# Performance work log

Hardware: AMD Instinct MI355X
Metric: run time of the kernel (lower is better)

Reference implementation:

```python
import jax, jax.numpy as jnp
import numpy as np
import math

B, T, C, H, S = 2, 2048, 1024, 16, 16
HD = C // H
EPS = 1e-5


def setup_inputs() -> dict:
    key = jax.random.key(0)
    ks = jax.random.split(key, 20)
    sc = 1.0 / math.sqrt(C)
    inp = {
        "x": jax.random.normal(ks[0], (B, T, C), jnp.float32),
        # A_log_fwd: log(arange(1..S)) repeated over dim (as in __init__)
        "A_log": jnp.log(jnp.tile(jnp.arange(1, S + 1, dtype=jnp.float32), (C, 1))),
        # Linear weights stored (in, out); apply as x @ W + b
        "Wd": jax.random.normal(ks[1], (C, C), jnp.float32) * sc,
        "bd": jnp.full((C,), -3.0, jnp.float32),
        "WB": jax.random.normal(ks[2], (C, S), jnp.float32) * sc,
        "WC": jax.random.normal(ks[3], (C, S), jnp.float32) * sc,
        "Wq": jax.random.normal(ks[4], (C, C), jnp.float32) * sc,
        "bq": jnp.zeros((C,), jnp.float32),
        "Wk": jax.random.normal(ks[5], (C, C), jnp.float32) * sc,
        "bk": jnp.zeros((C,), jnp.float32),
        "Wv": jax.random.normal(ks[6], (C, C), jnp.float32) * sc,
        "bv": jnp.zeros((C,), jnp.float32),
        "Wx": jax.random.normal(ks[7], (C, C), jnp.float32) * sc,
        "bx": jnp.zeros((C,), jnp.float32),
        "Wo": jax.random.normal(ks[8], (C, C), jnp.float32) * sc,
        "bo": jnp.zeros((C,), jnp.float32),
        "ln_g": jnp.ones((C,), jnp.float32),
        "ln_b": jnp.zeros((C,), jnp.float32),
        "temp": jnp.full((1, H, 1, 1), 0.5, jnp.float32),
    }
    return inp


def _forward(x, A_log, Wd, bd, WB, WC, Wq, bq, Wk, bk, Wv, bv, Wx, bx, Wo, bo, ln_g, ln_b, temp):
    x_base = x @ Wx + bx                      # (B,T,C)
    delta = jax.nn.softplus(x @ Wd + bd)      # (B,T,C)
    B_mat = x @ WB                            # (B,T,S)
    C_mat = x @ WC                            # (B,T,S)
    A = -jnp.exp(A_log)                       # (C,S)

    def scan_fn(h, inp):
        xb_t, d_t, B_t, C_t = inp             # (B,C),(B,C),(B,S),(B,S)
        bar_A = jnp.exp(d_t[..., None] * A)   # (B,C,S)
        h = bar_A * h + (d_t * xb_t)[..., None] * B_t[:, None, :]
        y = jnp.einsum('bcs,bs->bc', h, C_t)
        return h, y

    h0 = jnp.zeros((B, C, S), x.dtype)
    xs = (jnp.swapaxes(x_base, 0, 1), jnp.swapaxes(delta, 0, 1),
          jnp.swapaxes(B_mat, 0, 1), jnp.swapaxes(C_mat, 0, 1))
    _, ys = jax.lax.scan(scan_fn, h0, xs)
    out_fwd = jnp.swapaxes(ys, 0, 1)          # (B,T,C)

    # LayerNorm(x_base + out_fwd)
    hyb = x_base + out_fwd
    mu = hyb.mean(-1, keepdims=True)
    var = hyb.var(-1, keepdims=True)
    hybrid = (hyb - mu) * jax.lax.rsqrt(var + EPS) * ln_g + ln_b

    def heads(W, b):
        return (hybrid @ W + b).reshape(B, T, H, HD).transpose(0, 2, 1, 3)

    Q, K, V = heads(Wq, bq), heads(Wk, bk), heads(Wv, bv)
    scores = jnp.einsum('bhqd,bhkd->bhqk', Q, K) / math.sqrt(HD)
    scores = scores * jax.nn.softplus(temp)
    mask = jnp.tril(jnp.ones((T, T), bool))
    scores = jnp.where(mask[None, None], scores, -jnp.inf)
    attn = jax.nn.softmax(scores, axis=-1)
    out = jnp.einsum('bhqk,bhkd->bhqd', attn, V).transpose(0, 2, 1, 3).reshape(B, T, C)
    return out @ Wo + bo


def reference(x, A_log, Wd, bd, WB, WC, Wq, bq, Wk, bk, Wv, bv, Wx, bx, Wo, bo, ln_g, ln_b, temp):
    return _forward(x, A_log, Wd, bd, WB, WC, Wq, bq, Wk, bk, Wv, bv, Wx, bx, Wo, bo, ln_g, ln_b, temp)
```

## Files before the change

### kernel.cpp

```cpp
#include <hip/hip_runtime.h>
#include <math.h>

#define B_  2
#define T_  2048
#define C_  1024
#define H_  16
#define S_  16
#define HD_ 64
#define NCH 32
#define CHL 64

typedef short  short8  __attribute__((ext_vector_type(8)));
typedef unsigned short ushort8 __attribute__((ext_vector_type(8)));
typedef unsigned short ushort4v __attribute__((ext_vector_type(4)));
typedef float  f32x4   __attribute__((ext_vector_type(4)));

__device__ __forceinline__ float softplus_f(float v) {
    return fmaxf(v, 0.f) + log1pf(__expf(-fabsf(v)));
}

__device__ __forceinline__ unsigned short f2bf(float x) {
    unsigned u = __float_as_uint(x);
    u += 0x7fffu + ((u >> 16) & 1u);
    return (unsigned short)(u >> 16);
}

__device__ __forceinline__ void gload16(const unsigned short* g,
                                        unsigned short* l)
{
    __builtin_amdgcn_global_load_lds(
        (const __attribute__((address_space(1))) unsigned int*)g,
        (__attribute__((address_space(3))) unsigned int*)l, 16, 0, 0);
}

__global__ __launch_bounds__(256) void cast_bf16(const float* __restrict__ in,
                                                 unsigned short* __restrict__ out,
                                                 int n4)
{
    int i = blockIdx.x * 256 + threadIdx.x;
    if (i >= n4) return;
    float4 v = ((const float4*)in)[i];
    ushort4v o = {f2bf(v.x), f2bf(v.y), f2bf(v.z), f2bf(v.w)};
    ((ushort4v*)out)[i] = o;
}

__device__ __forceinline__ void wtrans_body(const float* __restrict__ W,
                                            unsigned short* __restrict__ WT,
                                            int bx, int by, int tid)
{
    __shared__ float t[32][33];
    const int n0 = bx * 32, k0 = by * 32;
    const int tx = tid & 31, ty = tid >> 5;
#pragma unroll
    for (int p = 0; p < 4; ++p)
        t[ty + p * 8][tx] = W[(size_t)(k0 + ty + p * 8) * C_ + n0 + tx];
    __syncthreads();
#pragma unroll
    for (int p = 0; p < 4; ++p)
        WT[(size_t)(n0 + ty + p * 8) * C_ + k0 + tx] = f2bf(t[tx][ty + p * 8]);
}

__global__ __launch_bounds__(256) void wtrans(const float* __restrict__ W,
                                              unsigned short* __restrict__ WT)
{
    wtrans_body(W, WT, blockIdx.x, blockIdx.y, threadIdx.x);
}

__global__ __launch_bounds__(256) void wtrans_multi(
    const float* __restrict__ Wx, const float* __restrict__ Wd,
    const float* __restrict__ Wq, const float* __restrict__ Wk,
    const float* __restrict__ Wv,
    unsigned short* __restrict__ Astack, unsigned short* __restrict__ Wqkv)
{
    const float* src;
    unsigned short* dst;
    switch (blockIdx.z) {
        case 0: src = Wx; dst = Astack; break;
        case 1: src = Wd; dst = Astack + (size_t)1024 * 1024; break;
        case 2: src = Wq; dst = Wqkv; break;
        case 3: src = Wk; dst = Wqkv + (size_t)1024 * 1024; break;
        default: src = Wv; dst = Wqkv + (size_t)2048 * 1024; break;
    }
    wtrans_body(src, dst, blockIdx.x, blockIdx.y, threadIdx.x);
}

__global__ __launch_bounds__(256) void prep_misc(
    const float* __restrict__ WB, const float* __restrict__ WC,
    const float* __restrict__ bx, const float* __restrict__ bd,
    const float* __restrict__ bq, const float* __restrict__ bk,
    const float* __restrict__ bv,
    unsigned short* __restrict__ Astack, float* __restrict__ biasPD,
    float* __restrict__ biasQKV)
{
    int gid = blockIdx.x * 256 + threadIdx.x;
    if (gid < 32768) {
        int w = gid >> 14, rem = gid & 16383;
        int s = rem >> 10, k = rem & 1023;
        const float* src = w ? WC : WB;
        Astack[(size_t)(2048 + w * 16 + s) * 1024 + k] = f2bf(src[k * 16 + s]);
    } else {
        int id = gid - 32768;
        if (id < 2176) {
            biasPD[id] = id < 1024 ? bx[id] : (id < 2048 ? bd[id - 1024] : 0.f);
        } else {
            int id2 = id - 2176;
            if (id2 < 3072)
                biasQKV[id2] = id2 < 1024 ? bq[id2]
                             : (id2 < 2048 ? bk[id2 - 1024] : bv[id2 - 2048]);
        }
    }
}

__global__ __launch_bounds__(256) void gemm_mfma(
    const unsigned short* __restrict__ A, const unsigned short* __restrict__ Bm,
    const float* __restrict__ bias,
    void* __restrict__ outv, void* __restrict__ out2,
    void* __restrict__ out3, void* __restrict__ out4,
    int M, int N, int K, int lda, int mode)
{
    __shared__ __align__(16) unsigned short As[4][4096];
    __shared__ __align__(16) unsigned short Bs[4][4096];

    const int tid = threadIdx.x;
    const int w = tid >> 6, lane = tid & 63;
    const int lq = lane & 15, lg = lane >> 4;
    const int wm = w >> 1, wn = w & 1;
    const int mBase = blockIdx.y * 128, nBase = blockIdx.x * 128;

    const int c0 = tid, c1 = tid + 256;
    const int rA0 = ((c0 >> 6) << 4) + (c0 & 15), kO0 = ((c0 >> 4) & 3) << 3;
    const int rA1 = ((c1 >> 6) << 4) + (c1 & 15), kO1 = ((c1 >> 4) & 3) << 3;

    const int wL0 = w * 512;
    const int wL1 = 2048 + w * 512;

    f32x4 acc[4][4];
#pragma unroll
    for (int i = 0; i < 4; ++i)
#pragma unroll
        for (int j = 0; j < 4; ++j) acc[i][j] = (f32x4){0.f, 0.f, 0.f, 0.f};

    const unsigned short* ga0 = A  + (size_t)(mBase + rA0) * lda + kO0;
    const unsigned short* ga1 = A  + (size_t)(mBase + rA1) * lda + kO1;
    const unsigned short* gb0 = Bm + (size_t)(nBase + rA0) * lda + kO0;
    const unsigned short* gb1 = Bm + (size_t)(nBase + rA1) * lda + kO1;

    #define STAGE(bufv, k0v)                               \
        do {                                               \
            gload16(ga0 + (k0v), &As[bufv][wL0]);          \
            gload16(ga1 + (k0v), &As[bufv][wL1]);          \
            gload16(gb0 + (k0v), &Bs[bufv][wL0]);          \
            gload16(gb1 + (k0v), &Bs[bufv][wL1]);          \
        } while (0)
    #define COMPUTE(bufv)                                                       \
        do {                                                                    \
            short8 a[4], b[4];                                                  \
            _Pragma("unroll")                                                   \
            for (int i = 0; i < 4; ++i)                                         \
                a[i] = *(const short8*)&As[bufv][((wm * 4 + i) * 64 + lg * 16 + lq) * 8]; \
            _Pragma("unroll")                                                   \
            for (int j = 0; j < 4; ++j)                                         \
                b[j] = *(const short8*)&Bs[bufv][((wn * 4 + j) * 64 + lg * 16 + lq) * 8]; \
            _Pragma("unroll")                                                   \
            for (int i = 0; i < 4; ++i)                                         \
                _Pragma("unroll")                                               \
                for (int j = 0; j < 4; ++j)                                     \
                    acc[i][j] = __builtin_amdgcn_mfma_f32_16x16x32_bf16(        \
                        a[i], b[j], acc[i][j], 0, 0, 0);                        \
        } while (0)
    #define WAITV4() asm volatile("s_waitcnt vmcnt(4)" ::: "memory")
    #define WAITV0() asm volatile("s_waitcnt vmcnt(0)" ::: "memory")
    #define LGKM0()  asm volatile("s_waitcnt lgkmcnt(0)" ::: "memory")
    #define STEP(cbuf, kt)                                          \
        do {                                                        \
            if ((kt) + 32 < K) WAITV4(); else WAITV0();             \
            LGKM0();                                                \
            __builtin_amdgcn_s_barrier();                           \
            if ((kt) + 64 < K) STAGE(((cbuf) + 2) & 3, (kt) + 64);  \
            COMPUTE(cbuf);                                          \
        } while (0)

    STAGE(0, 0);
    STAGE(1, 32);

    for (int k0 = 0; k0 < K; k0 += 128) {
        STEP(0, k0);
        STEP(1, k0 + 32);
        STEP(2, k0 + 64);
        STEP(3, k0 + 96);
    }
    #undef STAGE
    #undef COMPUTE
    #undef WAITV4
    #undef WAITV0
    #undef LGKM0
    #undef STEP

    if (mode == 0) {
        float* O = (float*)outv;
#pragma unroll
        for (int j = 0; j < 4; ++j) {
            int Cg = nBase + wn * 64 + j * 16 + lq;
            float bb = bias[Cg];
#pragma unroll
            for (int i = 0; i < 4; ++i) {
                int Rb = mBase + wm * 64 + i * 16 + lg * 4;
#pragma unroll
                for (int r = 0; r < 4; ++r)
                    O[(size_t)(Rb + r) * N + Cg] = acc[i][j][r] + bb;
            }
        }
    } else {
        float* xbaseT = (float*)outv;
        float* deltaT = (float*)out2;
        float* BmT    = (float*)out3;
        float* CmT    = (float*)out4;
#pragma unroll
        for (int i = 0; i < 4; ++i) {
            int Rb = mBase + wm * 64 + i * 16 + lg * 4;
            if (Rb >= 2080) continue;
            float bb[4];
#pragma unroll
            for (int r = 0; r < 4; ++r) bb[r] = bias[Rb + r];
#pragma unroll
            for (int j = 0; j < 4; ++j) {
                int Cg = nBase + wn * 64 + j * 16 + lq;
                int b = Cg >> 11, t = Cg & (T_ - 1);
#pragma unroll
                for (int r = 0; r < 4; ++r) {
                    int R = Rb + r;
                    float v = acc[i][j][r] + bb[r];
                    if (Rb < 1024) {
                        xbaseT[((size_t)b * C_ + R) * T_ + t] = v;
                    } else if (Rb < 2048) {
                        deltaT[((size_t)b * C_ + (R - 1024)) * T_ + t] =
                            softplus_f(v);
                    } else if (Rb < 2064) {
                        BmT[((size_t)b * S_ + (R - 2048)) * T_ + t] = v;
                    } else {
                        CmT[((size_t)b * S_ + (R - 2064)) * T_ + t] = v;
                    }
                }
            }
        }
    }
}

__global__ __launch_bounds__(512, 2) void gemm_mfma256(
    const unsigned short* __restrict__ A, const unsigned short* __restrict__ Bm,
    const float* __restrict__ bias,
    void* __restrict__ outv, void* __restrict__ out2,
    void* __restrict__ out3,
    int M, int N, int K, int lda)
{
    __shared__ __align__(16) unsigned short AS[2][2][8192];
    __shared__ __align__(16) unsigned short BS[2][2][8192];

    const int tid = threadIdx.x;
    const int w = tid >> 6, lane = tid & 63;
    const int lq = lane & 15, lg = lane >> 4;
    const int wm = w >> 2, wn = w & 3;
    const int mBase = blockIdx.y * 256, nBase = blockIdx.x * 256;

    const int c0 = tid, c1 = tid + 512;
    const int r0 = ((c0 >> 6) << 4) | (c0 & 15), k0l = ((c0 >> 4) & 3) << 3;
    const int r1 = ((c1 >> 6) << 4) | (c1 & 15), k1l = ((c1 >> 4) & 3) << 3;
    const unsigned short* gA0 = A  + (size_t)(mBase + r0) * lda + k0l;
    const unsigned short* gA1 = A  + (size_t)(mBase + r1) * lda + k1l;
    const unsigned short* gB0 = Bm + (size_t)(nBase + r0) * lda + k0l;
    const unsigned short* gB1 = Bm + (size_t)(nBase + r1) * lda + k1l;

    f32x4 acc[8][4];
#pragma unroll
    for (int i = 0; i < 8; ++i)
#pragma unroll
        for (int j = 0; j < 4; ++j) acc[i][j] = (f32x4){0.f, 0.f, 0.f, 0.f};

    #define STG_A(buf_, half_, kb_)                                           \
        do {                                                                  \
            gload16(gA0 + (kb_) + (half_) * 32, &AS[buf_][half_][c0 * 8]);    \
            gload16(gA1 + (kb_) + (half_) * 32, &AS[buf_][half_][c1 * 8]);    \
        } while (0)
    #define STG_B(buf_, half_, kb_)                                           \
        do {                                                                  \
            gload16(gB0 + (kb_) + (half_) * 32, &BS[buf_][half_][c0 * 8]);    \
            gload16(gB1 + (kb_) + (half_) * 32, &BS[buf_][half_][c1 * 8]);    \
        } while (0)
    #define WAITV8() asm volatile("s_waitcnt vmcnt(8)" ::: "memory")
    #define WAITV4() asm volatile("s_waitcnt vmcnt(4)" ::: "memory")
    #define WAITV0() asm volatile("s_waitcnt vmcnt(0)" ::: "memory")

    #define PHASE(buf_, half_, qi_, STAGE_STMT, GATE_STMT)                    \
        do {                                                                  \
            short8 a_[4];                                                     \
            _Pragma("unroll")                                                 \
            for (int i = 0; i < 4; ++i)                                       \
                a_[i] = *(const short8*)&AS[buf_][half_]                      \
                    [((wm * 8 + (qi_) * 4 + i) * 64 + lg * 16 + lq) * 8];     \
            if ((qi_) == 0) {                                                 \
                _Pragma("unroll")                                             \
                for (int j = 0; j < 4; ++j)                                   \
                    bfr[j] = *(const short8*)&BS[buf_][half_]                 \
                        [((wn * 4 + j) * 64 + lg * 16 + lq) * 8];             \
            }                                                                 \
            STAGE_STMT;                                                       \
            __builtin_amdgcn_s_barrier();                                     \
            asm volatile("s_waitcnt lgkmcnt(0)" ::: "memory");                \
            __builtin_amdgcn_s_setprio(1);                                    \
            _Pragma("unroll")                                                 \
            for (int i = 0; i < 4; ++i)                                       \
                _Pragma("unroll")                                             \
                for (int j = 0; j < 4; ++j)                                   \
                    acc[(qi_) * 4 + i][j] =                                   \
                        __builtin_amdgcn_mfma_f32_16x16x32_bf16(              \
                            a_[i], bfr[j], acc[(qi_) * 4 + i][j], 0, 0, 0);   \
            __builtin_amdgcn_s_setprio(0);                                    \
            GATE_STMT;                                                        \
            __builtin_amdgcn_s_barrier();                                     \
        } while (0)

    STG_A(0, 0, 0);
    STG_B(0, 0, 0);
    STG_A(0, 1, 0);
    STG_B(0, 1, 0);
    STG_A(1, 0, 64);
    STG_B(1, 0, 64);
    WAITV8();
    __builtin_amdgcn_s_barrier();

    const int NT = K >> 6;
    for (int kt = 0; kt < NT; ++kt) {
        const int buf = kt & 1, nbuf = buf ^ 1;
        const int kb1 = (kt + 1) << 6, kb2 = (kt + 2) << 6;
        short8 bfr[4];
        PHASE(buf, 0, 0, { if (kt + 1 < NT) STG_A(nbuf, 1, kb1); }, {});
        PHASE(buf, 0, 1, { if (kt + 1 < NT) STG_B(nbuf, 1, kb1); },
              { if (kt < NT - 1) WAITV8(); else WAITV0(); });
        PHASE(buf, 1, 0, { if (kt + 2 < NT) STG_A(buf, 0, kb2); }, {});
        PHASE(buf, 1, 1, { if (kt + 2 < NT) STG_B(buf, 0, kb2); },
              { if (kt < NT - 2) WAITV8();
                else if (kt == NT - 2) WAITV4(); });
    }
    #undef STG_A
    #undef STG_B
    #undef WAITV8
    #undef WAITV4
    #undef WAITV0
    #undef PHASE

    unsigned short* Qb  = (unsigned short*)outv;
    unsigned short* Kb  = (unsigned short*)out2;
    unsigned short* VTb = (unsigned short*)out3;
#pragma unroll
    for (int j = 0; j < 4; ++j) {
        int Cg = nBase + wn * 64 + j * 16 + lq;
        int reg = Cg >> 10, c = Cg & 1023;
        int h = c >> 6, hd = c & 63;
        float bb = bias[Cg];
#pragma unroll
        for (int i = 0; i < 8; ++i) {
            int Rb = mBase + wm * 128 + i * 16 + lg * 4;
#pragma unroll
            for (int r = 0; r < 4; ++r) {
                int R = Rb + r, b = R >> 11, t = R & (T_ - 1);
                unsigned short o = f2bf(acc[i][j][r] + bb);
                if (reg == 0)
                    Qb[(((size_t)(b * H_ + h) * T_ + t) * HD_) + hd] = o;
                else if (reg == 1)
                    Kb[(((size_t)(b * H_ + h) * T_ + t) * HD_) + hd] = o;
                else
                    VTb[(((size_t)(b * H_ + h) * HD_ + hd) * T_) + t] = o;
            }
        }
    }
}

__global__ __launch_bounds__(256) void scan_partial(
    const float* __restrict__ xbaseT, const float* __restrict__ deltaT,
    const float* __restrict__ BmT, const float* __restrict__ A_log,
    float4* __restrict__ Pbuf, float4* __restrict__ Lbuf)
{
    const int tid = threadIdx.x;
    const int s4 = tid & 3;
    const int cm = tid >> 2;
    const int cg = blockIdx.x & 15;
    const int k  = (blockIdx.x >> 4) & (NCH - 1);
    const int b  = blockIdx.x >> 9;
    const int c  = cg * 64 + cm;

    float a[4];
#pragma unroll
    for (int j = 0; j < 4; ++j)
        a[j] = -__expf(A_log[c * S_ + s4 * 4 + j]);

    const int tb = k * CHL;
    const float* dp = deltaT + ((size_t)b * C_ + c) * T_ + tb;
    const float* xp = xbaseT + ((size_t)b * C_ + c) * T_ + tb;
    const float* bp = BmT + ((size_t)(b * S_ + s4 * 4)) * T_ + tb;

    float L[4] = {0.f, 0.f, 0.f, 0.f};
    float sumd = 0.f;
    for (int t0 = 0; t0 < CHL; t0 += 4) {
        float4 d4 = *(const float4*)&dp[t0];
        float4 x4 = *(const float4*)&xp[t0];
        float dv[4] = {d4.x, d4.y, d4.z, d4.w};
        float xv[4] = {x4.x, x4.y, x4.z, x4.w};
        float bv[4][4];
#pragma unroll
        for (int j = 0; j < 4; ++j) {
            float4 b4 = *(const float4*)&bp[(size_t)j * T_ + t0];
            bv[j][0] = b4.x; bv[j][1] = b4.y; bv[j][2] = b4.z; bv[j][3] = b4.w;
        }
#pragma unroll
        for (int q = 0; q < 4; ++q) {
            float u = dv[q] * xv[q];
            sumd += dv[q];
#pragma unroll
            for (int j = 0; j < 4; ++j)
                L[j] = fmaf(__expf(dv[q] * a[j]), L[j], u * bv[j][q]);
        }
    }
    int gid = blockIdx.x * 256 + tid;
    float4 P4 = {__expf(a[0] * sumd), __expf(a[1] * sumd),
                 __expf(a[2] * sumd), __expf(a[3] * sumd)};
    float4 L4 = {L[0], L[1], L[2], L[3]};
    Pbuf[gid] = P4;
    Lbuf[gid] = L4;
}

__global__ __launch_bounds__(256) void scan_final(
    const float* __restrict__ xbaseT, const float* __restrict__ deltaT,
    const float* __restrict__ BmT, const float* __restrict__ CmT,
    const float* __restrict__ A_log, const float4* __restrict__ Pbuf,
    const float4* __restrict__ Lbuf, float* __restrict__ hyb)
{
    const int tid = threadIdx.x;
    const int s4 = tid & 3;
    const int cm = tid >> 2;
    const int cg = blockIdx.x & 15;
    const int k  = (blockIdx.x >> 4) & (NCH - 1);
    const int b  = blockIdx.x >> 9;
    const int c  = cg * 64 + cm;

    float h[4] = {0.f, 0.f, 0.f, 0.f};
    for (int k2 = 0; k2 < k; ++k2) {
        int gid2 = (((b * NCH + k2) << 4) + cg) * 256 + tid;
        float4 P4 = Pbuf[gid2];
        float4 L4 = Lbuf[gid2];
        h[0] = fmaf(P4.x, h[0], L4.x);
        h[1] = fmaf(P4.y, h[1], L4.y);
        h[2] = fmaf(P4.z, h[2], L4.z);
        h[3] = fmaf(P4.w, h[3], L4.w);
    }

    float a[4];
#pragma unroll
    for (int j = 0; j < 4; ++j)
        a[j] = -__expf(A_log[c * S_ + s4 * 4 + j]);

    const int tb = k * CHL;
    const float* dp = deltaT + ((size_t)b * C_ + c) * T_ + tb;
    const float* xp = xbaseT + ((size_t)b * C_ + c) * T_ + tb;
    const float* bp = BmT + ((size_t)(b * S_ + s4 * 4)) * T_ + tb;
    const float* cp = CmT + ((size_t)(b * S_ + s4 * 4)) * T_ + tb;
    float* hp = hyb + ((size_t)b * T_ + tb) * C_ + c;

    for (int t0 = 0; t0 < CHL; t0 += 4) {
        float4 d4 = *(const float4*)&dp[t0];
        float4 x4 = *(const float4*)&xp[t0];
        float dv[4] = {d4.x, d4.y, d4.z, d4.w};
        float xv[4] = {x4.x, x4.y, x4.z, x4.w};
        float bv[4][4], cv[4][4];
#pragma unroll
        for (int j = 0; j < 4; ++j) {
            float4 b4 = *(const float4*)&bp[(size_t)j * T_ + t0];
            float4 c4 = *(const float4*)&cp[(size_t)j * T_ + t0];
            bv[j][0] = b4.x; bv[j][1] = b4.y; bv[j][2] = b4.z; bv[j][3] = b4.w;
            cv[j][0] = c4.x; cv[j][1] = c4.y; cv[j][2] = c4.z; cv[j][3] = c4.w;
        }
#pragma unroll
        for (int q = 0; q < 4; ++q) {
            float u = dv[q] * xv[q];
#pragma unroll
            for (int j = 0; j < 4; ++j)
                h[j] = fmaf(__expf(dv[q] * a[j]), h[j], u * bv[j][q]);
            float y = h[0] * cv[0][q];
            y = fmaf(h[1], cv[1][q], y);
            y = fmaf(h[2], cv[2][q], y);
            y = fmaf(h[3], cv[3][q], y);
            y += __shfl_xor(y, 1, 64);
            y += __shfl_xor(y, 2, 64);
            if (s4 == 0) hp[(size_t)(t0 + q) * C_] = xv[q] + y;
        }
    }
}

__global__ __launch_bounds__(256) void layernorm_kernel(
    const float* __restrict__ in, const float* __restrict__ g,
    const float* __restrict__ beta, unsigned short* __restrict__ out)
{
    const int row = blockIdx.x;
    const float* rp = in + (size_t)row * C_;
    const int c = threadIdx.x * 4;
    float4 v = *(const float4*)&rp[c];
    float sum = v.x + v.y + v.z + v.w;
    float sq = v.x * v.x + v.y * v.y + v.z * v.z + v.w * v.w;
#pragma unroll
    for (int off = 1; off < 64; off <<= 1) {
        sum += __shfl_xor(sum, off, 64);
        sq += __shfl_xor(sq, off, 64);
    }
    __shared__ float sS[4], sQ[4];
    int wave = threadIdx.x >> 6, lane = threadIdx.x & 63;
    if (lane == 0) { sS[wave] = sum; sQ[wave] = sq; }
    __syncthreads();
    sum = sS[0] + sS[1] + sS[2] + sS[3];
    sq = sQ[0] + sQ[1] + sQ[2] + sQ[3];
    const float mu = sum * (1.f / C_);
    const float var = sq * (1.f / C_) - mu * mu;
    const float rstd = rsqrtf(var + 1e-5f);
    float4 gg = *(const float4*)&g[c];
    float4 bb = *(const float4*)&beta[c];
    ushort4v o;
    o.x = f2bf((v.x - mu) * rstd * gg.x + bb.x);
    o.y = f2bf((v.y - mu) * rstd * gg.y + bb.y);
    o.z = f2bf((v.z - mu) * rstd * gg.z + bb.z);
    o.w = f2bf((v.w - mu) * rstd * gg.w + bb.w);
    *(ushort4v*)&out[(size_t)row * C_ + c] = o;
}

#define BKT 128
#define KP  72
#define VP  136
__global__ __launch_bounds__(256) void attn_mfma(
    const unsigned short* __restrict__ Q, const unsigned short* __restrict__ K,
    const unsigned short* __restrict__ VT, const float* __restrict__ temp,
    unsigned short* __restrict__ out)
{
    __shared__ __align__(16) unsigned short Ks[BKT * KP];
    __shared__ __align__(16) unsigned short Vs[80 * VP];
    __shared__ __align__(16) unsigned short Ps[64 * VP];

    const int tid = threadIdx.x;
    const int w = tid >> 6, lane = tid & 63;
    const int lq = lane & 15, lg = lane >> 4;
    const int p  = blockIdx.x & 15;
    const int bh = blockIdx.x >> 4;
    const int b = bh >> 4, h = bh & 15;

    const float scale = softplus_f(temp[h]) * 0.125f;
    const unsigned short* Qp = Q + (size_t)bh * T_ * HD_;
    const unsigned short* Kp = K + (size_t)bh * T_ * HD_;
    const unsigned short* Vp = VT + (size_t)bh * HD_ * T_;

    {
        int r = 64 + (tid >> 4), o = (tid & 15) * 8;
        ushort8 ones = {0x3f80, 0x3f80, 0x3f80, 0x3f80,
                        0x3f80, 0x3f80, 0x3f80, 0x3f80};
        *(ushort8*)&Vs[r * VP + o] = ones;
    }

    ushort8 kreg[4], vreg[4];
    #define LOADKV(jtv)                                                        \
        do {                                                                   \
            int kb = (jtv) * BKT;                                              \
            _Pragma("unroll")                                                  \
            for (int q2 = 0; q2 < 4; ++q2) {                                   \
                int c = tid + q2 * 256;                                        \
                kreg[q2] = *(const ushort8*)&Kp[(size_t)(kb + (c >> 3)) * HD_  \
                                                + (c & 7) * 8];                \
                vreg[q2] = *(const ushort8*)&Vp[(size_t)(c >> 4) * T_ + kb     \
                                                + (c & 15) * 8];               \
            }                                                                  \
        } while (0)

    for (int half = 0; half < 2; ++half) {
        const int qi = half ? p : (31 - p);
        const int qbase = qi * 64;
        const int nT = (qbase + 64 + BKT - 1) / BKT;

        short8 qf[2];
#pragma unroll
        for (int s = 0; s < 2; ++s)
            qf[s] = *(const short8*)&Qp[(size_t)(qbase + w * 16 + lq) * HD_
                                        + s * 32 + lg * 8];
        LOADKV(0);

        float m_i[4];
        f32x4 o[5];
#pragma unroll
        for (int r = 0; r < 4; ++r) m_i[r] = -INFINITY;
#pragma unroll
        for (int j = 0; j < 5; ++j) o[j] = (f32x4){0.f, 0.f, 0.f, 0.f};

        for (int jt = 0; jt < nT; ++jt) {
            const int kbase = jt * BKT;
            const bool last = (jt == nT - 1);
            __syncthreads();
#pragma unroll
            for (int q2 = 0; q2 < 4; ++q2) {
                int c = tid + q2 * 256;
                *(ushort8*)&Ks[(c >> 3) * KP + (c & 7) * 8] = kreg[q2];
                *(ushort8*)&Vs[(c >> 4) * VP + (c & 15) * 8] = vreg[q2];
            }
            __syncthreads();
            if (jt + 1 < nT) LOADKV(jt + 1);

            f32x4 sacc[8];
#pragma unroll
            for (int j = 0; j < 8; ++j) sacc[j] = (f32x4){0.f, 0.f, 0.f, 0.f};
#pragma unroll
            for (int s = 0; s < 2; ++s) {
#pragma unroll
                for (int j = 0; j < 8; ++j) {
                    short8 kf = *(const short8*)&Ks[(j * 16 + lq) * KP
                                                    + s * 32 + lg * 8];
                    sacc[j] = __builtin_amdgcn_mfma_f32_16x16x32_bf16(
                        qf[s], kf, sacc[j], 0, 0, 0);
                }
            }

#pragma unroll
            for (int r = 0; r < 4; ++r) {
                int qrow = qbase + w * 16 + lg * 4 + r;
                float sv[8];
#pragma unroll
                for (int j = 0; j < 8; ++j) {
                    sv[j] = sacc[j][r] * scale;
                    if (last && (kbase + j * 16 + lq > qrow)) sv[j] = -INFINITY;
                }
                float mx = sv[0];
#pragma unroll
                for (int j = 1; j < 8; ++j) mx = fmaxf(mx, sv[j]);
                mx = fmaxf(mx, __shfl_xor(mx, 1, 64));
                mx = fmaxf(mx, __shfl_xor(mx, 2, 64));
                mx = fmaxf(mx, __shfl_xor(mx, 4, 64));
                mx = fmaxf(mx, __shfl_xor(mx, 8, 64));
                float mnew = fmaxf(m_i[r], mx);
                float alpha = __expf(m_i[r] - mnew);
                m_i[r] = mnew;
#pragma unroll
                for (int j = 0; j < 5; ++j) o[j][r] *= alpha;
#pragma unroll
                for (int j = 0; j < 8; ++j)
                    Ps[(w * 16 + lg * 4 + r) * VP + j * 16 + lq] =
                        f2bf(__expf(sv[j] - mnew));
            }

#pragma unroll
            for (int s2 = 0; s2 < 4; ++s2) {
                short8 pf = *(const short8*)&Ps[(w * 16 + lq) * VP
                                                + s2 * 32 + lg * 8];
#pragma unroll
                for (int j = 0; j < 5; ++j) {
                    short8 vf = *(const short8*)&Vs[(j * 16 + lq) * VP
                                                    + s2 * 32 + lg * 8];
                    o[j] = __builtin_amdgcn_mfma_f32_16x16x32_bf16(
                        pf, vf, o[j], 0, 0, 0);
                }
            }
        }

#pragma unroll
        for (int r = 0; r < 4; ++r) {
            float inv = 1.f / o[4][r];
            int qrow = qbase + w * 16 + lg * 4 + r;
#pragma unroll
            for (int j = 0; j < 4; ++j)
                out[((size_t)(b * T_ + qrow)) * C_ + h * 64 + j * 16 + lq] =
                    f2bf(o[j][r] * inv);
        }
    }
    #undef LOADKV
}

extern "C" void kernel_launch(void* const* d_in, const int* in_sizes, int n_in,
                              void* d_out, int out_size, void* d_ws, size_t ws_size,
                              hipStream_t stream)
{
    const float* x     = (const float*)d_in[0];
    const float* A_log = (const float*)d_in[1];
    const float* Wd    = (const float*)d_in[2];
    const float* bd    = (const float*)d_in[3];
    const float* WB    = (const float*)d_in[4];
    const float* WC    = (const float*)d_in[5];
    const float* Wq    = (const float*)d_in[6];
    const float* bq    = (const float*)d_in[7];
    const float* Wk    = (const float*)d_in[8];
    const float* bk    = (const float*)d_in[9];
    const float* Wv    = (const float*)d_in[10];
    const float* bv    = (const float*)d_in[11];
    const float* Wx    = (const float*)d_in[12];
    const float* bx    = (const float*)d_in[13];
    const float* Wo    = (const float*)d_in[14];
    const float* bo    = (const float*)d_in[15];
    const float* ln_g  = (const float*)d_in[16];
    const float* ln_b  = (const float*)d_in[17];
    const float* temp  = (const float*)d_in[18];

    char* wsb = (char*)d_ws;
    const size_t MB = 1024 * 1024;
    const size_t HMB = 512 * 1024;
    unsigned short* xb      = (unsigned short*)(wsb);
    float4* Pbuf            = (float4*)(wsb);
    float4* Lbuf            = (float4*)(wsb + 4 * MB);
    unsigned short* hybrid  = (unsigned short*)(wsb);
    unsigned short* Astack  = (unsigned short*)(wsb + 8 * MB);
    float* biasPD           = (float*)(wsb + 8 * MB + (size_t)2176 * 2048);
    float* biasQKV          = biasPD + 2176;
    unsigned short* WqkvT   = (unsigned short*)(wsb + 12 * MB + HMB);
    unsigned short* WoT     = (unsigned short*)(wsb + 18 * MB + HMB);
    float* deltaT           = (float*)(wsb + 18 * MB + HMB);
    float* xbaseT           = (float*)(wsb + 34 * MB + HMB);
    float* hyb              = (float*)(wsb + 50 * MB + HMB);
    float* BmT              = (float*)(wsb + 66 * MB + HMB);
    float* CmT              = BmT + (size_t)B_ * S_ * T_;
    unsigned short* Qb      = (unsigned short*)(wsb + 20 * MB + HMB);
    unsigned short* Kb      = (unsigned short*)(wsb + 28 * MB + HMB);
    unsigned short* VTb     = (unsigned short*)(wsb + 36 * MB + HMB);
    unsigned short* attnO   = (unsigned short*)(wsb + 44 * MB + HMB);

    cast_bf16<<<4096, 256, 0, stream>>>(x, xb, (B_ * T_ * C_) / 4);
    wtrans_multi<<<dim3(32, 32, 5), 256, 0, stream>>>(Wx, Wd, Wq, Wk, Wv,
                                                      Astack, WqkvT);
    prep_misc<<<149, 256, 0, stream>>>(WB, WC, bx, bd, bq, bk, bv,
                                       Astack, biasPD, biasQKV);

    gemm_mfma<<<dim3(32, 17, 1), 256, 0, stream>>>(
        Astack, xb, biasPD, xbaseT, deltaT, BmT, CmT,
        2176, 4096, 1024, 1024, 1);

    const int scanBlocks = B_ * NCH * (C_ / 64);
    scan_partial<<<scanBlocks, 256, 0, stream>>>(xbaseT, deltaT, BmT, A_log,
                                                 Pbuf, Lbuf);
    scan_final<<<scanBlocks, 256, 0, stream>>>(xbaseT, deltaT, BmT, CmT, A_log,
                                               Pbuf, Lbuf, hyb);

    layernorm_kernel<<<B_ * T_, 256, 0, stream>>>(hyb, ln_g, ln_b, hybrid);

    gemm_mfma256<<<dim3(12, 16, 1), 512, 0, stream>>>(
        hybrid, WqkvT, biasQKV, Qb, Kb, VTb,
        4096, 3072, 1024, 1024);

    attn_mfma<<<B_ * H_ * 16, 256, 0, stream>>>(Qb, Kb, VTb, temp, attnO);

    wtrans<<<dim3(32, 32), 256, 0, stream>>>(Wo, WoT);
    gemm_mfma<<<dim3(8, 32, 1), 256, 0, stream>>>(
        attnO, WoT, bo, d_out, nullptr, nullptr, nullptr,
        4096, 1024, 1024, 1024, 0);
}
```

Before: 457.4 us.

## Add dedicated 128x256 pipelined GEMM kernel for input projection with transposed outputs

```diff
diff --git a/kernel.cpp b/kernel.cpp
--- a/kernel.cpp
+++ b/kernel.cpp
@@ -114,9 +114,8 @@
 __global__ __launch_bounds__(256) void gemm_mfma(
     const unsigned short* __restrict__ A, const unsigned short* __restrict__ Bm,
     const float* __restrict__ bias,
-    void* __restrict__ outv, void* __restrict__ out2,
-    void* __restrict__ out3, void* __restrict__ out4,
-    int M, int N, int K, int lda, int mode)
+    void* __restrict__ outv,
+    int M, int N, int K, int lda)
 {
     __shared__ __align__(16) unsigned short As[4][4096];
     __shared__ __align__(16) unsigned short Bs[4][4096];
@@ -196,50 +195,135 @@
     #undef LGKM0
     #undef STEP
 
-    if (mode == 0) {
-        float* O = (float*)outv;
+    float* O = (float*)outv;
+#pragma unroll
+    for (int j = 0; j < 4; ++j) {
+        int Cg = nBase + wn * 64 + j * 16 + lq;
+        float bb = bias[Cg];
+#pragma unroll
+        for (int i = 0; i < 4; ++i) {
+            int Rb = mBase + wm * 64 + i * 16 + lg * 4;
+#pragma unroll
+            for (int r = 0; r < 4; ++r)
+                O[(size_t)(Rb + r) * N + Cg] = acc[i][j][r] + bb;
+        }
+    }
+}
+
+__global__ __launch_bounds__(512, 2) void gemm_projT(
+    const unsigned short* __restrict__ A, const unsigned short* __restrict__ Bm,
+    const float* __restrict__ bias,
+    float* __restrict__ xbaseT, float* __restrict__ deltaT,
+    float* __restrict__ BmT, float* __restrict__ CmT,
+    int K, int lda)
+{
+    __shared__ __align__(16) unsigned short AS[2][2][4096];
+    __shared__ __align__(16) unsigned short BS[2][2][8192];
+
+    const int tid = threadIdx.x;
+    const int w = tid >> 6, lane = tid & 63;
+    const int lq = lane & 15, lg = lane >> 4;
+    const int wm = w >> 2, wn = w & 3;
+    const int mBase = blockIdx.y * 128, nBase = blockIdx.x * 256;
+
+    const int rA = ((tid >> 6) << 4) | (tid & 15);
+    const int kA = ((tid >> 4) & 3) << 3;
+    const unsigned short* gA = A + (size_t)(mBase + rA) * lda + kA;
+    const int eA = tid * 8;
+    const int c0 = tid, c1 = tid + 512;
+    const int rB0 = ((c0 >> 6) << 4) | (c0 & 15), kB0 = ((c0 >> 4) & 3) << 3;
+    const int rB1 = ((c1 >> 6) << 4) | (c1 & 15), kB1 = ((c1 >> 4) & 3) << 3;
+    const unsigned short* gB0 = Bm + (size_t)(nBase + rB0) * lda + kB0;
+    const unsigned short* gB1 = Bm + (size_t)(nBase + rB1) * lda + kB1;
+
+    f32x4 acc[4][4];
+#pragma unroll
+    for (int i = 0; i < 4; ++i)
+#pragma unroll
+        for (int j = 0; j < 4; ++j) acc[i][j] = (f32x4){0.f, 0.f, 0.f, 0.f};
+
+    #define STG(buf_, half_, kb_)                                             \
+        do {                                                                  \
+            gload16(gA  + (kb_) + (half_) * 32, &AS[buf_][half_][eA]);        \
+            gload16(gB0 + (kb_) + (half_) * 32, &BS[buf_][half_][c0 * 8]);    \
+            gload16(gB1 + (kb_) + (half_) * 32, &BS[buf_][half_][c1 * 8]);    \
+        } while (0)
+    #define WAITV6() asm volatile("s_waitcnt vmcnt(6)" ::: "memory")
+    #define WAITV3() asm volatile("s_waitcnt vmcnt(3)" ::: "memory")
+    #define WAITV0() asm volatile("s_waitcnt vmcnt(0)" ::: "memory")
+
+    #define PHASE(buf_, half_, STAGE_STMT, GATE_STMT)                         \
+        do {                                                                  \
+            short8 a_[4], b_[4];                                              \
+            _Pragma("unroll")                                                 \
+            for (int i = 0; i < 4; ++i)                                       \
+                a_[i] = *(const short8*)&AS[buf_][half_]                      \
+                    [((wm * 4 + i) * 64 + lg * 16 + lq) * 8];                 \
+            _Pragma("unroll")                                                 \
+            for (int j = 0; j < 4; ++j)                                       \
+                b_[j] = *(const short8*)&BS[buf_][half_]                      \
+                    [((wn * 4 + j) * 64 + lg * 16 + lq) * 8];                 \
+            STAGE_STMT;                                                       \
+            __builtin_amdgcn_s_barrier();                                     \
+            asm volatile("s_waitcnt lgkmcnt(0)" ::: "memory");                \
+            __builtin_amdgcn_s_setprio(1);                                    \
+            _Pragma("unroll")                                                 \
+            for (int i = 0; i < 4; ++i)                                       \
+                _Pragma("unroll")                                             \
+                for (int j = 0; j < 4; ++j)                                   \
+                    acc[i][j] = __builtin_amdgcn_mfma_f32_16x16x32_bf16(      \
+                        a_[i], b_[j], acc[i][j], 0, 0, 0);                    \
+            __builtin_amdgcn_s_setprio(0);                                    \
+            GATE_STMT;                                                        \
+            __builtin_amdgcn_s_barrier();                                     \
+        } while (0)
+
+    STG(0, 0, 0);
+    STG(0, 1, 0);
+    STG(1, 0, 64);
+    WAITV6();
+    __builtin_amdgcn_s_barrier();
+
+    const int NT = K >> 6;
+    for (int kt = 0; kt < NT; ++kt) {
+        const int buf = kt & 1, nbuf = buf ^ 1;
+        const int kb1 = (kt + 1) << 6, kb2 = (kt + 2) << 6;
+        PHASE(buf, 0, { if (kt + 1 < NT) STG(nbuf, 1, kb1); },
+              { if (kt < NT - 1) WAITV6(); else WAITV3(); });
+        PHASE(buf, 1, { if (kt + 2 < NT) STG(buf, 0, kb2); },
+              { if (kt < NT - 2) WAITV6();
+                else if (kt == NT - 2) WAITV3(); else WAITV0(); });
+    }
+    #undef STG
+    #undef WAITV6
+    #undef WAITV3
+    #undef WAITV0
+    #undef PHASE
+
+#pragma unroll
+    for (int i = 0; i < 4; ++i) {
+        int Rb = mBase + wm * 64 + i * 16 + lg * 4;
+        if (Rb >= 2080) continue;
+        float bb[4];
+#pragma unroll
+        for (int r = 0; r < 4; ++r) bb[r] = bias[Rb + r];
 #pragma unroll
         for (int j = 0; j < 4; ++j) {
             int Cg = nBase + wn * 64 + j * 16 + lq;
-            float bb = bias[Cg];
-#pragma unroll
-            for (int i = 0; i < 4; ++i) {
-                int Rb = mBase + wm * 64 + i * 16 + lg * 4;
-#pragma unroll
-                for (int r = 0; r < 4; ++r)
-                    O[(size_t)(Rb + r) * N + Cg] = acc[i][j][r] + bb;
-            }
-        }
-    } else {
-        float* xbaseT = (float*)outv;
-        float* deltaT = (float*)out2;
-        float* BmT    = (float*)out3;
-        float* CmT    = (float*)out4;
-#pragma unroll
-        for (int i = 0; i < 4; ++i) {
-            int Rb = mBase + wm * 64 + i * 16 + lg * 4;
-            if (Rb >= 2080) continue;
-            float bb[4];
-#pragma unroll
-            for (int r = 0; r < 4; ++r) bb[r] = bias[Rb + r];
-#pragma unroll
-            for (int j = 0; j < 4; ++j) {
-                int Cg = nBase + wn * 64 + j * 16 + lq;
-                int b = Cg >> 11, t = Cg & (T_ - 1);
-#pragma unroll
-                for (int r = 0; r < 4; ++r) {
-                    int R = Rb + r;
-                    float v = acc[i][j][r] + bb[r];
-                    if (Rb < 1024) {
-                        xbaseT[((size_t)b * C_ + R) * T_ + t] = v;
-                    } else if (Rb < 2048) {
-                        deltaT[((size_t)b * C_ + (R - 1024)) * T_ + t] =
-                            softplus_f(v);
-                    } else if (Rb < 2064) {
-                        BmT[((size_t)b * S_ + (R - 2048)) * T_ + t] = v;
-                    } else {
-                        CmT[((size_t)b * S_ + (R - 2064)) * T_ + t] = v;
-                    }
+            int b = Cg >> 11, t = Cg & (T_ - 1);
+#pragma unroll
+            for (int r = 0; r < 4; ++r) {
+                int R = Rb + r;
+                float v = acc[i][j][r] + bb[r];
+                if (Rb < 1024) {
+                    xbaseT[((size_t)b * C_ + R) * T_ + t] = v;
+                } else if (Rb < 2048) {
+                    deltaT[((size_t)b * C_ + (R - 1024)) * T_ + t] =
+                        softplus_f(v);
+                } else if (Rb < 2064) {
+                    BmT[((size_t)b * S_ + (R - 2048)) * T_ + t] = v;
+                } else {
+                    CmT[((size_t)b * S_ + (R - 2064)) * T_ + t] = v;
                 }
             }
         }
@@ -726,9 +810,9 @@
     prep_misc<<<149, 256, 0, stream>>>(WB, WC, bx, bd, bq, bk, bv,
                                        Astack, biasPD, biasQKV);
 
-    gemm_mfma<<<dim3(32, 17, 1), 256, 0, stream>>>(
+    gemm_projT<<<dim3(16, 17, 1), 512, 0, stream>>>(
         Astack, xb, biasPD, xbaseT, deltaT, BmT, CmT,
-        2176, 4096, 1024, 1024, 1);
+        1024, 1024);
 
     const int scanBlocks = B_ * NCH * (C_ / 64);
     scan_partial<<<scanBlocks, 256, 0, stream>>>(xbaseT, deltaT, BmT, A_log,
@@ -746,6 +830,6 @@
 
     wtrans<<<dim3(32, 32), 256, 0, stream>>>(Wo, WoT);
     gemm_mfma<<<dim3(8, 32, 1), 256, 0, stream>>>(
-        attnO, WoT, bo, d_out, nullptr, nullptr, nullptr,
-        4096, 1024, 1024, 1024, 0);
-}
+        attnO, WoT, bo, d_out,
+        4096, 1024, 1024, 1024);
+}
```

Measured after the change: 453.5 us. Within noise of the previous version (-0.9%).
